# Performance work log

Hardware: AMD Instinct MI355X
Metric: run time of the kernel (lower is better)

The kernel has to match this reference:

```python
import jax, jax.numpy as jnp
import numpy as np

D_MODEL = 2048
N_EXPERTS = 64


def setup_inputs() -> dict:
    key = jax.random.key(0)
    kx, kw = jax.random.split(key)
    x = jax.random.normal(kx, (4, 4096, D_MODEL), dtype=jnp.float32)
    # nn.Linear(d_model, n_experts, bias=False): weight [n_experts, d_model]
    W = jax.random.normal(kw, (N_EXPERTS, D_MODEL), dtype=jnp.float32) * (1.0 / np.sqrt(D_MODEL))
    return {"x": x, "W": W, "n_active": 2, "capacity": 4096}


def reference(x, W, n_active, capacity):
    # router_logits = x @ W^T : [b, s, e]
    router_logits = jnp.einsum("bsd,ed->bse", x, W)
    router_probs = jax.nn.softmax(router_logits, axis=-1)
    # top-k over experts
    scores, expert_indices = jax.lax.top_k(router_probs, n_active)  # [b, s, k]
    scores = scores / jnp.sum(scores, axis=-1, keepdims=True)
    n_experts = router_probs.shape[-1]
    # scatter normalized scores into dense gate tensor [b, s, e]
    # (top-k indices are distinct, so one-hot sum == torch scatter_)
    gates = jnp.sum(
        jax.nn.one_hot(expert_indices, n_experts, dtype=scores.dtype) * scores[..., None],
        axis=-2,
    )
    expert_counts = jnp.sum(gates, axis=(0, 1))  # [e]
    load_loss = jnp.mean((expert_counts / jnp.sum(expert_counts) * n_experts - 1.0) ** 2)
    return gates, expert_indices, load_loss
```

## Files before the change

### kernel.cpp

```cpp
#include <hip/hip_runtime.h>
#include <hip/hip_bf16.h>
#include <math.h>

#define TOK_TOTAL 16384
#define D_MODEL   2048
#define NEXP      64
#define BM        64
#define KC        32
#define KHALF     1024
#define NCH       (KHALF / KC)
#define PAD       40
#define TAU       1e-3f

#define IDX_OFF   (TOK_TOTAL * NEXP)
#define LOSS_OFF  (IDX_OFF + TOK_TOTAL * 2)

#define WS_CNT    (TOK_TOTAL * NEXP)
#define WS_RCNT   (WS_CNT + TOK_TOTAL)
#define WS_RLIST  (WS_RCNT + 1)

typedef __attribute__((ext_vector_type(8))) short short8_t;
typedef __attribute__((ext_vector_type(4))) float f32x4;

__global__ __launch_bounds__(256, 4)
void router_gemm(const float* __restrict__ x, const float* __restrict__ W,
                 float* __restrict__ p0, float* __restrict__ p1,
                 int* __restrict__ rep_cnt)
{
    __shared__ __align__(16) short lds[2][4][BM][PAD];

    const int t  = threadIdx.x;
    const int w  = t >> 6;
    const int l  = t & 63;
    const int kh = blockIdx.x & 1;
    const long tok0 = (long)(blockIdx.x >> 1) * BM;
    const long kb0  = (long)kh * KHALF;

    if (blockIdx.x == 0 && t == 0) *rep_cnt = 0;

    const int sr = t >> 3;
    const int sc = (t & 7) * 4;

    f32x4 acc[4];
    #pragma unroll
    for (int nt = 0; nt < 4; ++nt) acc[nt] = (f32x4){0.f, 0.f, 0.f, 0.f};

    float4 xr[2], wr[2];

    auto LOADCH = [&](int ic) {
        const long k0 = kb0 + (long)ic * KC;
        #pragma unroll
        for (int p = 0; p < 2; ++p) {
            xr[p] = *(const float4*)(x + (tok0 + sr + 32 * p) * D_MODEL + k0 + sc);
            wr[p] = *(const float4*)(W + (long)(sr + 32 * p) * D_MODEL + k0 + sc);
        }
    };

    auto STORECH = [&](int buf) {
        #pragma unroll
        for (int p = 0; p < 2; ++p) {
            const int row = sr + 32 * p;
            const float fx[4] = {xr[p].x, xr[p].y, xr[p].z, xr[p].w};
            const float fw[4] = {wr[p].x, wr[p].y, wr[p].z, wr[p].w};
            short xh[4], xl[4], wh[4], wl[4];
            #pragma unroll
            for (int j = 0; j < 4; ++j) {
                __hip_bfloat16 h = __float2bfloat16(fx[j]);
                xh[j] = __builtin_bit_cast(short, h);
                xl[j] = __builtin_bit_cast(short, __float2bfloat16(fx[j] - __bfloat162float(h)));
                __hip_bfloat16 g = __float2bfloat16(fw[j]);
                wh[j] = __builtin_bit_cast(short, g);
                wl[j] = __builtin_bit_cast(short, __float2bfloat16(fw[j] - __bfloat162float(g)));
            }
            *(short4*)(&lds[buf][0][row][sc]) = make_short4(xh[0], xh[1], xh[2], xh[3]);
            *(short4*)(&lds[buf][1][row][sc]) = make_short4(xl[0], xl[1], xl[2], xl[3]);
            *(short4*)(&lds[buf][2][row][sc]) = make_short4(wh[0], wh[1], wh[2], wh[3]);
            *(short4*)(&lds[buf][3][row][sc]) = make_short4(wl[0], wl[1], wl[2], wl[3]);
        }
    };

    auto COMPUTE = [&](int buf) {
        const int arow = w * 16 + (l & 15);
        const int ke   = (l >> 4) * 8;
        short8_t ah = *(const short8_t*)(&lds[buf][0][arow][ke]);
        short8_t al = *(const short8_t*)(&lds[buf][1][arow][ke]);
        #pragma unroll
        for (int nt = 0; nt < 4; ++nt) {
            const int brow = nt * 16 + (l & 15);
            short8_t bh = *(const short8_t*)(&lds[buf][2][brow][ke]);
            short8_t bl = *(const short8_t*)(&lds[buf][3][brow][ke]);
            acc[nt] = __builtin_amdgcn_mfma_f32_16x16x32_bf16(ah, bl, acc[nt], 0, 0, 0);
            acc[nt] = __builtin_amdgcn_mfma_f32_16x16x32_bf16(al, bh, acc[nt], 0, 0, 0);
            acc[nt] = __builtin_amdgcn_mfma_f32_16x16x32_bf16(ah, bh, acc[nt], 0, 0, 0);
        }
    };

    LOADCH(0);
    STORECH(0);
    __syncthreads();

    for (int ic = 0; ic < NCH; ++ic) {
        const int buf = ic & 1;
        const bool pre = (ic + 1 < NCH);
        if (pre) LOADCH(ic + 1);
        COMPUTE(buf);
        if (pre) STORECH(buf ^ 1);
        __syncthreads();
    }

    float* dst = kh ? p1 : p0;
    #pragma unroll
    for (int nt = 0; nt < 4; ++nt)
        #pragma unroll
        for (int r = 0; r < 4; ++r)
            dst[(tok0 + w * 16 + (l >> 4) * 4 + r) * NEXP + nt * 16 + (l & 15)] = acc[nt][r];
}

__global__ __launch_bounds__(256, 1)
void router_combine(const float* __restrict__ p0, const float* __restrict__ p1,
                    float* __restrict__ out, float* __restrict__ cntp,
                    int* __restrict__ rep_cnt, int* __restrict__ rep_list)
{
    __shared__ float4 s_ig[64];
    const int t = threadIdx.x;
    const int r = t >> 2, q = t & 3;
    const long tok0 = (long)blockIdx.x * 64;
    const long tok  = tok0 + r;

    float v[16];
    {
        const float4* a4 = (const float4*)(p0 + tok * NEXP) + q * 4;
        const float4* b4 = (const float4*)(p1 + tok * NEXP) + q * 4;
        #pragma unroll
        for (int j = 0; j < 4; ++j) {
            float4 a = a4[j], b = b4[j];
            v[j*4+0] = a.x + b.x; v[j*4+1] = a.y + b.y;
            v[j*4+2] = a.z + b.z; v[j*4+3] = a.w + b.w;
        }
    }

    float b0 = -1e30f, b1 = -1e30f, b2 = -1e30f;
    int i0 = 0, i1 = 0;
    const int ebase = q * 16;
    #pragma unroll
    for (int j = 0; j < 16; ++j) {
        float xv = v[j]; int e = ebase + j;
        if (xv > b0)      { b2 = b1; b1 = b0; i1 = i0; b0 = xv; i0 = e; }
        else if (xv > b1) { b2 = b1; b1 = xv; i1 = e; }
        else if (xv > b2) { b2 = xv; }
    }

    #pragma unroll
    for (int d = 1; d <= 2; d <<= 1) {
        float ob0 = __shfl_xor(b0, d, 64), ob1 = __shfl_xor(b1, d, 64), ob2 = __shfl_xor(b2, d, 64);
        int   oi0 = __shfl_xor(i0, d, 64), oi1 = __shfl_xor(i1, d, 64);
        bool a0w = (b0 > ob0) || (b0 == ob0 && i0 < oi0);
        float nb0 = a0w ? b0 : ob0;  int ni0 = a0w ? i0 : oi0;
        float ca  = a0w ? b1 : ob1;  int cia = a0w ? i1 : oi1;
        float cb  = a0w ? ob0 : b0;  int cib = a0w ? oi0 : i0;
        float wa2 = a0w ? b2 : ob2;
        float lb1 = a0w ? ob1 : b1;
        bool w1 = (ca > cb) || (ca == cb && cia < cib);
        float nb1 = w1 ? ca : cb;  int ni1 = w1 ? cia : cib;
        float nb2 = w1 ? fmaxf(wa2, cb) : fmaxf(ca, lb1);
        b0 = nb0; i0 = ni0; b1 = nb1; i1 = ni1; b2 = nb2;
    }

    float ex = __expf(b1 - b0);
    float g0 = 1.f / (1.f + ex);
    float g1 = ex * g0;

    {
        float* orow = out + tok * NEXP + ebase;
        #pragma unroll
        for (int j4 = 0; j4 < 4; ++j4) {
            float gv[4];
            #pragma unroll
            for (int j = 0; j < 4; ++j) {
                int e = ebase + j4 * 4 + j;
                gv[j] = (e == i0) ? g0 : ((e == i1) ? g1 : 0.f);
            }
            *(float4*)(orow + j4 * 4) = make_float4(gv[0], gv[1], gv[2], gv[3]);
        }
    }

    if (q == 0) {
        out[IDX_OFF + 2 * tok]     = (float)i0;
        out[IDX_OFF + 2 * tok + 1] = (float)i1;
        s_ig[r] = make_float4((float)i0, (float)i1, g0, g1);
        if ((b0 - b1 < TAU) || (b1 - b2 < TAU)) {
            int p = atomicAdd(rep_cnt, 1);
            rep_list[p] = (int)tok;
        }
    }
    __syncthreads();

    if (t < 64) {
        float c = 0.f;
        for (int tt = 0; tt < 64; ++tt) {
            float4 gg = s_ig[tt];
            if ((int)gg.x == t) c += gg.z;
            if ((int)gg.y == t) c += gg.w;
        }
        cntp[blockIdx.x * NEXP + t] = c;
    }
}

__global__ __launch_bounds__(256, 1)
void router_tail(const float* __restrict__ x, const float* __restrict__ W,
                 float* __restrict__ out, const float* __restrict__ cntp,
                 const int* __restrict__ rep_cnt, const int* __restrict__ rep_list)
{
    const int t = threadIdx.x;

    if (blockIdx.x == 0) {
        __shared__ double red[4][NEXP];
        const int e = t & 63, p = t >> 6;
        double s = 0.0;
        for (int b = 0; b < 64; ++b)
            s += (double)cntp[(p * 64 + b) * NEXP + e];
        red[p][e] = s;
        __syncthreads();
        if (t == 0) {
            double sc[NEXP], tot = 0.0;
            for (int i = 0; i < NEXP; ++i) {
                sc[i] = red[0][i] + red[1][i] + red[2][i] + red[3][i];
                tot += sc[i];
            }
            double loss = 0.0;
            for (int i = 0; i < NEXP; ++i) {
                double d = sc[i] / tot * (double)NEXP - 1.0;
                loss += d * d;
            }
            out[LOSS_OFF] = (float)(loss / NEXP);
        }
        return;
    }

    __shared__ double red[4][NEXP];
    const int nf = *rep_cnt;
    const int e = t & 63, part = t >> 6;
    for (int i = (int)blockIdx.x - 1; i < nf; i += (int)gridDim.x - 1) {
        const long tok = rep_list[i];
        const float* xr = x + tok * D_MODEL;
        const float* wr = W + (long)e * D_MODEL;
        const int k0 = part * 512;
        double s = 0.0;
        for (int kk = 0; kk < 512; kk += 4) {
            float4 xv = *(const float4*)(xr + k0 + kk);
            float4 wv = *(const float4*)(wr + k0 + kk);
            s = fma((double)xv.x, (double)wv.x, s);
            s = fma((double)xv.y, (double)wv.y, s);
            s = fma((double)xv.z, (double)wv.z, s);
            s = fma((double)xv.w, (double)wv.w, s);
        }
        red[part][e] = s;
        __syncthreads();
        if (t == 0) {
            double best = -1e300, sec = -1e300;
            int bi = 0, si = 0;
            for (int ee = 0; ee < NEXP; ++ee) {
                double vv = red[0][ee] + red[1][ee] + red[2][ee] + red[3][ee];
                if (vv > best)     { sec = best; si = bi; best = vv; bi = ee; }
                else if (vv > sec) { sec = vv; si = ee; }
            }
            out[IDX_OFF + 2 * tok]     = (float)bi;
            out[IDX_OFF + 2 * tok + 1] = (float)si;
        }
        __syncthreads();
    }
}

extern "C" void kernel_launch(void* const* d_in, const int* in_sizes, int n_in,
                              void* d_out, int out_size, void* d_ws, size_t ws_size,
                              hipStream_t stream)
{
    const float* x = (const float*)d_in[0];
    const float* W = (const float*)d_in[1];
    float* out  = (float*)d_out;
    float* ws   = (float*)d_ws;
    float* p0   = out;
    float* p1   = ws;
    float* cntp = ws + WS_CNT;
    int*   rep_cnt  = (int*)(ws + WS_RCNT);
    int*   rep_list = (int*)(ws + WS_RLIST);

    router_gemm   <<<(TOK_TOTAL / BM) * 2, 256, 0, stream>>>(x, W, p0, p1, rep_cnt);
    router_combine<<<TOK_TOTAL / 64, 256, 0, stream>>>(p0, p1, out, cntp, rep_cnt, rep_list);
    router_tail   <<<257, 256, 0, stream>>>(x, W, out, cntp, rep_cnt, rep_list);
}
```

Before: 83.87 us.

## Pre-split W into bf16 hi/lo MFMA layout and drop LDS staging in GEMM

Adds a small kernel that converts W once per call into bf16 high/low parts, stored in a fragment-friendly layout in workspace. The GEMM then loads x straight into registers in MFMA operand order, converts on the fly, and reads the W fragments from global/L2 without LDS or __syncthreads. This is meant to remove the repeated per-block W conversion, the LDS traffic and the barriers. In exchange it adds an extra kernel launch, relies on cache hits for W reads, and runs with less latency hiding, since prefetch is only one chunk deep and occupancy is lower.

```diff
diff --git a/kernel.cpp b/kernel.cpp
--- a/kernel.cpp
+++ b/kernel.cpp
@@ -5,107 +5,89 @@
 #define TOK_TOTAL 16384
 #define D_MODEL   2048
 #define NEXP      64
-#define BM        64
-#define KC        32
-#define KHALF     1024
-#define NCH       (KHALF / KC)
-#define PAD       40
+#define KQ        1024
+#define NCHQ      (KQ / 32)
 #define TAU       1e-3f
 
 #define IDX_OFF   (TOK_TOTAL * NEXP)
 #define LOSS_OFF  (IDX_OFF + TOK_TOTAL * 2)
 
-#define WS_CNT    (TOK_TOTAL * NEXP)
-#define WS_RCNT   (WS_CNT + TOK_TOTAL)
+#define WS_WH     (TOK_TOTAL * NEXP)
+#define WS_WL     (WS_WH + 65536)
+#define WS_CNTP   (WS_WL + 65536)
+#define WS_RCNT   (WS_CNTP + 16384)
 #define WS_RLIST  (WS_RCNT + 1)
 
 typedef __attribute__((ext_vector_type(8))) short short8_t;
 typedef __attribute__((ext_vector_type(4))) float f32x4;
 
-__global__ __launch_bounds__(256, 4)
-void router_gemm(const float* __restrict__ x, const float* __restrict__ W,
-                 float* __restrict__ p0, float* __restrict__ p1,
-                 int* __restrict__ rep_cnt)
-{
-    __shared__ __align__(16) short lds[2][4][BM][PAD];
-
-    const int t  = threadIdx.x;
-    const int w  = t >> 6;
-    const int l  = t & 63;
+__device__ inline void cvt_hl(float4 a, float4 b, short8_t& h8, short8_t& l8)
+{
+    const float f[8] = {a.x, a.y, a.z, a.w, b.x, b.y, b.z, b.w};
+    #pragma unroll
+    for (int j = 0; j < 8; ++j) {
+        __hip_bfloat16 h = __float2bfloat16(f[j]);
+        h8[j] = __builtin_bit_cast(short, h);
+        l8[j] = __builtin_bit_cast(short, __float2bfloat16(f[j] - __bfloat162float(h)));
+    }
+}
+
+__global__ __launch_bounds__(256, 1)
+void build_wt(const float* __restrict__ W, short8_t* __restrict__ WH8,
+              short8_t* __restrict__ WL8, int* __restrict__ rep_cnt)
+{
+    const int id = blockIdx.x * 256 + threadIdx.x;
+    if (id == 0) *rep_cnt = 0;
+    const int k8 = id & 255, e = id >> 8;
+    float4 a = *(const float4*)(W + (long)e * D_MODEL + k8 * 8);
+    float4 b = *(const float4*)(W + (long)e * D_MODEL + k8 * 8 + 4);
+    short8_t h8, l8;
+    cvt_hl(a, b, h8, l8);
+    WH8[k8 * NEXP + e] = h8;
+    WL8[k8 * NEXP + e] = l8;
+}
+
+__global__ __launch_bounds__(256, 2)
+void router_gemm(const float* __restrict__ x,
+                 const short8_t* __restrict__ WH8, const short8_t* __restrict__ WL8,
+                 float* __restrict__ p0, float* __restrict__ p1)
+{
+    const int t = threadIdx.x;
+    const int w = t >> 6, l = t & 63;
     const int kh = blockIdx.x & 1;
-    const long tok0 = (long)(blockIdx.x >> 1) * BM;
-    const long kb0  = (long)kh * KHALF;
-
-    if (blockIdx.x == 0 && t == 0) *rep_cnt = 0;
-
-    const int sr = t >> 3;
-    const int sc = (t & 7) * 4;
+    const long tokw = (long)(blockIdx.x >> 1) * 64 + w * 16;
+    const int lane16 = l & 15, kq = l >> 4;
+    const long kb0 = (long)kh * KQ;
+
+    const float* xp = x + (tokw + lane16) * D_MODEL + kb0 + kq * 8;
+    const short8_t* whp = WH8 + (kb0 / 8 + kq) * NEXP + lane16;
+    const short8_t* wlp = WL8 + (kb0 / 8 + kq) * NEXP + lane16;
 
     f32x4 acc[4];
     #pragma unroll
     for (int nt = 0; nt < 4; ++nt) acc[nt] = (f32x4){0.f, 0.f, 0.f, 0.f};
 
-    float4 xr[2], wr[2];
-
-    auto LOADCH = [&](int ic) {
-        const long k0 = kb0 + (long)ic * KC;
-        #pragma unroll
-        for (int p = 0; p < 2; ++p) {
-            xr[p] = *(const float4*)(x + (tok0 + sr + 32 * p) * D_MODEL + k0 + sc);
-            wr[p] = *(const float4*)(W + (long)(sr + 32 * p) * D_MODEL + k0 + sc);
-        }
-    };
-
-    auto STORECH = [&](int buf) {
-        #pragma unroll
-        for (int p = 0; p < 2; ++p) {
-            const int row = sr + 32 * p;
-            const float fx[4] = {xr[p].x, xr[p].y, xr[p].z, xr[p].w};
-            const float fw[4] = {wr[p].x, wr[p].y, wr[p].z, wr[p].w};
-            short xh[4], xl[4], wh[4], wl[4];
-            #pragma unroll
-            for (int j = 0; j < 4; ++j) {
-                __hip_bfloat16 h = __float2bfloat16(fx[j]);
-                xh[j] = __builtin_bit_cast(short, h);
-                xl[j] = __builtin_bit_cast(short, __float2bfloat16(fx[j] - __bfloat162float(h)));
-                __hip_bfloat16 g = __float2bfloat16(fw[j]);
-                wh[j] = __builtin_bit_cast(short, g);
-                wl[j] = __builtin_bit_cast(short, __float2bfloat16(fw[j] - __bfloat162float(g)));
-            }
-            *(short4*)(&lds[buf][0][row][sc]) = make_short4(xh[0], xh[1], xh[2], xh[3]);
-            *(short4*)(&lds[buf][1][row][sc]) = make_short4(xl[0], xl[1], xl[2], xl[3]);
-            *(short4*)(&lds[buf][2][row][sc]) = make_short4(wh[0], wh[1], wh[2], wh[3]);
-            *(short4*)(&lds[buf][3][row][sc]) = make_short4(wl[0], wl[1], wl[2], wl[3]);
-        }
-    };
-
-    auto COMPUTE = [&](int buf) {
-        const int arow = w * 16 + (l & 15);
-        const int ke   = (l >> 4) * 8;
-        short8_t ah = *(const short8_t*)(&lds[buf][0][arow][ke]);
-        short8_t al = *(const short8_t*)(&lds[buf][1][arow][ke]);
+    float4 xa = *(const float4*)(xp);
+    float4 xb = *(const float4*)(xp + 4);
+
+    #pragma unroll 2
+    for (int ic = 0; ic < NCHQ; ++ic) {
+        short8_t ah, al;
+        cvt_hl(xa, xb, ah, al);
+        if (ic + 1 < NCHQ) {
+            xa = *(const float4*)(xp + 32 * (ic + 1));
+            xb = *(const float4*)(xp + 32 * (ic + 1) + 4);
+        }
+        const short8_t* wh = whp + (long)ic * 4 * NEXP;
+        const short8_t* wl = wlp + (long)ic * 4 * NEXP;
         #pragma unroll
         for (int nt = 0; nt < 4; ++nt) {
-            const int brow = nt * 16 + (l & 15);
-            short8_t bh = *(const short8_t*)(&lds[buf][2][brow][ke]);
-            short8_t bl = *(const short8_t*)(&lds[buf][3][brow][ke]);
+            short8_t bh = wh[nt * 16];
+            short8_t bl = wl[nt * 16];
             acc[nt] = __builtin_amdgcn_mfma_f32_16x16x32_bf16(ah, bl, acc[nt], 0, 0, 0);
             acc[nt] = __builtin_amdgcn_mfma_f32_16x16x32_bf16(al, bh, acc[nt], 0, 0, 0);
             acc[nt] = __builtin_amdgcn_mfma_f32_16x16x32_bf16(ah, bh, acc[nt], 0, 0, 0);
         }
-    };
-
-    LOADCH(0);
-    STORECH(0);
-    __syncthreads();
-
-    for (int ic = 0; ic < NCH; ++ic) {
-        const int buf = ic & 1;
-        const bool pre = (ic + 1 < NCH);
-        if (pre) LOADCH(ic + 1);
-        COMPUTE(buf);
-        if (pre) STORECH(buf ^ 1);
-        __syncthreads();
     }
 
     float* dst = kh ? p1 : p0;
@@ -113,7 +95,7 @@
     for (int nt = 0; nt < 4; ++nt)
         #pragma unroll
         for (int r = 0; r < 4; ++r)
-            dst[(tok0 + w * 16 + (l >> 4) * 4 + r) * NEXP + nt * 16 + (l & 15)] = acc[nt][r];
+            dst[(tokw + kq * 4 + r) * NEXP + nt * 16 + lane16] = acc[nt][r];
 }
 
 __global__ __launch_bounds__(256, 1)
@@ -277,15 +259,18 @@
 {
     const float* x = (const float*)d_in[0];
     const float* W = (const float*)d_in[1];
-    float* out  = (float*)d_out;
-    float* ws   = (float*)d_ws;
-    float* p0   = out;
-    float* p1   = ws;
-    float* cntp = ws + WS_CNT;
-    int*   rep_cnt  = (int*)(ws + WS_RCNT);
-    int*   rep_list = (int*)(ws + WS_RLIST);
-
-    router_gemm   <<<(TOK_TOTAL / BM) * 2, 256, 0, stream>>>(x, W, p0, p1, rep_cnt);
+    float* out = (float*)d_out;
+    float* ws  = (float*)d_ws;
+    float* p0  = out;
+    float* p1  = ws;
+    short8_t* WH8 = (short8_t*)(ws + WS_WH);
+    short8_t* WL8 = (short8_t*)(ws + WS_WL);
+    float* cntp = ws + WS_CNTP;
+    int* rep_cnt  = (int*)(ws + WS_RCNT);
+    int* rep_list = (int*)(ws + WS_RLIST);
+
+    build_wt      <<<64, 256, 0, stream>>>(W, WH8, WL8, rep_cnt);
+    router_gemm   <<<(TOK_TOTAL / 64) * 2, 256, 0, stream>>>(x, WH8, WL8, p0, p1);
     router_combine<<<TOK_TOTAL / 64, 256, 0, stream>>>(p0, p1, out, cntp, rep_cnt, rep_list);
     router_tail   <<<257, 256, 0, stream>>>(x, W, out, cntp, rep_cnt, rep_list);
 }
```

New measurement: 83.73 us. About the same (-0.2%).
